# Kernel optimization log

Measured on AMD Instinct MI355X. Metric: run time of the kernel, lower is better.

Reference implementation:

```python
import jax, jax.numpy as jnp
import numpy as np

N = 100000      # nodes
E = 1600000     # edges (avg degree 16)
DIN = 128
DH = 128
DOUT = 16
G = 512         # graphs in batch


def setup_inputs() -> dict:
    key = jax.random.key(0)
    ks = jax.random.split(key, 12)
    def lin(k, fan_in, shape):
        return jax.random.uniform(k, shape, jnp.float32, -1.0, 1.0) / np.sqrt(fan_in)
    return {
        "x": jax.random.normal(ks[0], (N, DIN), jnp.float32),
        "edge_index": jax.random.randint(ks[1], (2, E), 0, N, jnp.int32),
        "edge_weight": jax.random.uniform(ks[2], (E,), jnp.float32),
        "batch": jnp.sort(jax.random.randint(ks[3], (N,), 0, G, jnp.int32)),
        "W1": lin(ks[4], DIN, (DIN, DH)), "b1": jnp.zeros((DH,), jnp.float32),
        "W2": lin(ks[5], DH, (DH, DH)),  "b2": jnp.zeros((DH,), jnp.float32),
        "W3": lin(ks[6], DH, (DH, DH)),  "b3": jnp.zeros((DH,), jnp.float32),
        "Wlin": lin(ks[7], DH, (DH, DOUT)), "blin": lin(ks[8], DH, (DOUT,)),
    }


def gcn_norm(edge_index, edge_weight, num_nodes):
    # PyG gcn_norm: add self-loops (weight 1), symmetric normalization
    loop = jnp.arange(num_nodes, dtype=edge_index.dtype)
    row = jnp.concatenate([edge_index[0], loop])
    col = jnp.concatenate([edge_index[1], loop])
    ew = jnp.concatenate([edge_weight, jnp.ones((num_nodes,), edge_weight.dtype)])
    deg = jax.ops.segment_sum(ew, col, num_segments=num_nodes)
    dinv = jnp.where(deg > 0, jax.lax.rsqrt(jnp.where(deg > 0, deg, 1.0)), 0.0)
    norm = dinv[row] * ew * dinv[col]
    return row, col, norm


def gcn_conv(x, W, b, row, col, norm, num_nodes):
    h = x @ W                                   # [N, d_out]
    msg = h[row] * norm[:, None]                # gather + scale  [E+N, d_out]
    out = jax.ops.segment_sum(msg, col, num_segments=num_nodes)
    return out + b


def reference(x, edge_index, edge_weight, batch, W1, b1, W2, b2, W3, b3, Wlin, blin):
    num_nodes = x.shape[0]
    row, col, norm = gcn_norm(edge_index, edge_weight, num_nodes)
    h = jax.nn.relu(gcn_conv(x, W1, b1, row, col, norm, num_nodes))
    h = jax.nn.relu(gcn_conv(h, W2, b2, row, col, norm, num_nodes))
    h = gcn_conv(h, W3, b3, row, col, norm, num_nodes)
    # global mean pool over graphs
    sums = jax.ops.segment_sum(h, batch, num_segments=G)          # [G, DH]
    cnt = jax.ops.segment_sum(jnp.ones((num_nodes,), h.dtype), batch, num_segments=G)
    hG = sums / jnp.maximum(cnt, 1.0)[:, None]
    # dropout is identity in eval mode
    return hG @ Wlin + blin
```

## Files before the change

kernel.cpp:

```cpp
#include <hip/hip_runtime.h>
#include <hip/hip_bf16.h>

#define NB 512
#define MAXBKT 512
#define PB 4

typedef __attribute__((ext_vector_type(8))) unsigned short ushort8;
typedef __attribute__((ext_vector_type(8))) short bf16x8;
typedef __attribute__((ext_vector_type(4))) float f32x4;

__device__ __forceinline__ unsigned short f2bf(float f) {
    unsigned u = __float_as_uint(f);
    unsigned r = (u + 0x7FFF + ((u >> 16) & 1)) >> 16;
    return (unsigned short)r;
}

__global__ __launch_bounds__(256) void k_wt3_hist(const float* __restrict__ W1,
                                                  const float* __restrict__ W2,
                                                  const float* __restrict__ W3,
                                                  const float* __restrict__ Wlin,
                                                  unsigned short* __restrict__ WT1,
                                                  unsigned short* __restrict__ WT2,
                                                  unsigned short* __restrict__ WLT,
                                                  const int* __restrict__ col, int E, int e2,
                                                  int per, int* __restrict__ cnt, int nbkt) {
    int b = blockIdx.x;
    if (b < 128) {
        const float* W = (b < 64) ? W1 : W2;
        unsigned short* WT = (b < 64) ? WT1 : WT2;
        int idx = (b & 63) * 256 + threadIdx.x;
        int nn = idx >> 7, k = idx & 127;
        WT[nn * 128 + k] = f2bf(W[k * 128 + nn]);
        return;
    }
    if (b < 136) {
        int idx = (b - 128) * 256 + threadIdx.x;
        int c = idx >> 7, k = idx & 127;
        float s = 0.f;
        for (int j = 0; j < 128; ++j) s += W3[k * 128 + j] * Wlin[j * 16 + c];
        WLT[c * 128 + k] = f2bf(s);
        return;
    }
    int hb = b - 136;
    __shared__ int h[MAXBKT];
    int t = threadIdx.x;
    for (int i = t; i < nbkt; i += 256) h[i] = 0;
    __syncthreads();
    int s = hb * per, e = min(s + per, e2);
    for (int i = s + t; i < e; i += 256) {
        int dst = (i < E) ? col[i] : i - E;
        atomicAdd(&h[dst >> 8], 1);
    }
    __syncthreads();
    for (int i = t; i < nbkt; i += 256) cnt[i * NB + hb] = h[i];
}

#define SCAN_T 256
#define SCAN_E 1024

__global__ void k_scan_a(const int* __restrict__ cnt, int n,
                         int* __restrict__ outp, int* __restrict__ bsum) {
    __shared__ int s[SCAN_T];
    int t = threadIdx.x, b = blockIdx.x;
    int base = b * SCAN_E + t * 4;
    int c0 = (base + 0 < n) ? cnt[base + 0] : 0;
    int c1 = (base + 1 < n) ? cnt[base + 1] : 0;
    int c2 = (base + 2 < n) ? cnt[base + 2] : 0;
    int c3 = (base + 3 < n) ? cnt[base + 3] : 0;
    int tsum = c0 + c1 + c2 + c3;
    s[t] = tsum; __syncthreads();
    for (int off = 1; off < SCAN_T; off <<= 1) {
        int v = (t >= off) ? s[t - off] : 0;
        __syncthreads();
        s[t] += v;
        __syncthreads();
    }
    int excl = s[t] - tsum;
    if (base + 0 < n) outp[base + 0] = excl;
    if (base + 1 < n) outp[base + 1] = excl + c0;
    if (base + 2 < n) outp[base + 2] = excl + c0 + c1;
    if (base + 3 < n) outp[base + 3] = excl + c0 + c1 + c2;
    if (t == 0) bsum[b] = s[SCAN_T - 1];
}

__global__ __launch_bounds__(256) void k_scan_b(int* __restrict__ bsum, int nb) {
    __shared__ int s[256];
    int t = threadIdx.x;
    int v = (t < nb) ? bsum[t] : 0;
    s[t] = v; __syncthreads();
    for (int off = 1; off < 256; off <<= 1) {
        int u = (t >= off) ? s[t - off] : 0;
        __syncthreads();
        s[t] += u;
        __syncthreads();
    }
    if (t < nb) bsum[t] = s[t] - v;
}

__global__ __launch_bounds__(256) void k_scatter1(const int* __restrict__ row,
                                                  const int* __restrict__ col,
                                                  const float* __restrict__ ew,
                                                  int E, int e2, int per,
                                                  const int* __restrict__ S,
                                                  const int* __restrict__ bsum,
                                                  uint2* __restrict__ csrR, int nbkt) {
    __shared__ int cur[MAXBKT];
    int t = threadIdx.x;
    for (int i = t; i < nbkt; i += 256) {
        int idx = i * NB + blockIdx.x;
        cur[i] = S[idx] + bsum[idx >> 10];
    }
    __syncthreads();
    int s = blockIdx.x * per, e = min(s + per, e2);
    for (int i = s + t; i < e; i += 256) {
        int src, dst; float w;
        if (i < E) { src = row[i]; dst = col[i]; w = ew[i]; }
        else       { src = dst = i - E; w = 1.0f; }
        int slot = atomicAdd(&cur[dst >> 8], 1);
        csrR[slot] = make_uint2(((unsigned)src << 8) | (unsigned)(dst & 255),
                                __float_as_uint(w));
    }
}

__global__ __launch_bounds__(256) void k_build(const uint2* __restrict__ csrR,
                                               const int* __restrict__ S,
                                               const int* __restrict__ bsum,
                                               int n, int e2,
                                               float2* __restrict__ csrF,
                                               float* __restrict__ dinv,
                                               int* __restrict__ rowptr, int nbkt) {
    __shared__ int   cnt[256];
    __shared__ float wsm[256];
    __shared__ int   off[256];
    __shared__ float dvs[256];
    __shared__ int   curs[256];
    int b = blockIdx.x, t = threadIdx.x;
    cnt[t] = 0; wsm[t] = 0.f;
    __syncthreads();
    int i0 = b * NB;
    int base = S[i0] + bsum[i0 >> 10];
    int end;
    if (b + 1 < nbkt) { int i1 = (b + 1) * NB; end = S[i1] + bsum[i1 >> 10]; }
    else end = e2;
    for (int i = base + t; i < end; i += 256) {
        uint2 r = csrR[i];
        int d = r.x & 255;
        atomicAdd(&cnt[d], 1);
        atomicAdd(&wsm[d], __uint_as_float(r.y));
    }
    __syncthreads();
    int   myc = cnt[t];
    float w   = wsm[t];
    float dv  = (w > 0.f) ? rsqrtf(w) : 0.f;
    dvs[t] = dv;
    off[t] = myc;
    __syncthreads();
    for (int o = 1; o < 256; o <<= 1) {
        int v = (t >= o) ? off[t - o] : 0;
        __syncthreads();
        off[t] += v;
        __syncthreads();
    }
    int excl = off[t] - myc;
    int node = b * 256 + t;
    if (node < n) { dinv[node] = dv; rowptr[node] = base + excl; }
    if (b == nbkt - 1 && t == 0) rowptr[n] = e2;
    curs[t] = excl;
    __syncthreads();
    for (int i = base + t; i < end; i += 256) {
        uint2 r = csrR[i];
        int d = r.x & 255;
        int src = (int)(r.x >> 8);
        int p = base + atomicAdd(&curs[d], 1);
        csrF[p] = make_float2(__int_as_float(src), __uint_as_float(r.y) * dvs[d]);
    }
}

__global__ __launch_bounds__(256) void k_gemm_mfma(const float* __restrict__ H,
                                                   const unsigned short* __restrict__ WT,
                                                   const float* __restrict__ dinv,
                                                   unsigned short* __restrict__ O, int n) {
    int wv = threadIdx.x >> 6, lane = threadIdx.x & 63;
    int rowBase = blockIdx.x * 64 + wv * 16;
    int lr = lane & 15;
    int lk = (lane >> 4) * 8;

    int arow = min(rowBase + lr, n - 1);
    bf16x8 a[4];
#pragma unroll
    for (int kk = 0; kk < 4; ++kk) {
        const float4* p = (const float4*)&H[(size_t)arow * 128 + kk * 32 + lk];
        float4 h0 = p[0], h1 = p[1];
        bf16x8 av;
        av[0] = (short)f2bf(h0.x); av[1] = (short)f2bf(h0.y);
        av[2] = (short)f2bf(h0.z); av[3] = (short)f2bf(h0.w);
        av[4] = (short)f2bf(h1.x); av[5] = (short)f2bf(h1.y);
        av[6] = (short)f2bf(h1.z); av[7] = (short)f2bf(h1.w);
        a[kk] = av;
    }

    f32x4 acc[8] = {};
#pragma unroll
    for (int c = 0; c < 8; ++c) {
#pragma unroll
        for (int kk = 0; kk < 4; ++kk) {
            bf16x8 b = *(const bf16x8*)&WT[(size_t)(c * 16 + lr) * 128 + kk * 32 + lk];
            acc[c] = __builtin_amdgcn_mfma_f32_16x16x32_bf16(a[kk], b, acc[c], 0, 0, 0);
        }
    }

#pragma unroll
    for (int r = 0; r < 4; ++r) {
        int node = rowBase + (lane >> 4) * 4 + r;
        if (node < n) {
            float sc = dinv[node];
#pragma unroll
            for (int c = 0; c < 8; ++c)
                O[(size_t)node * 128 + c * 16 + lr] = f2bf(acc[c][r] * sc);
        }
    }
}

#define AGG_BODY(BIAS)                                                          \
    int t = threadIdx.x;                                                        \
    int wv = t >> 6, lane = t & 63;                                             \
    int g = lane >> 4, sl = lane & 15;                                          \
    int node = blockIdx.x * 16 + wv * 4 + g;                                    \
    int s = 0, e = 0;                                                           \
    if (node < n) { s = rowptr[node]; e = rowptr[node + 1]; }                   \
    float a0 = 0.f, a1 = 0.f, a2 = 0.f, a3 = 0.f,                               \
          a4 = 0.f, a5 = 0.f, a6 = 0.f, a7 = 0.f;                               \
    int i = s;                                                                  \
    for (; i + 2 <= e; i += 2) {                                                \
        float2 p0 = csr[i], p1 = csr[i + 1];                                    \
        uint4 v0 = Hw[(size_t)__float_as_int(p0.x) * 16 + sl];                  \
        uint4 v1 = Hw[(size_t)__float_as_int(p1.x) * 16 + sl];                  \
        FMA8(v0, p0.y); FMA8(v1, p1.y);                                         \
    }                                                                           \
    if (i < e) {                                                                \
        float2 pp = csr[i];                                                     \
        uint4 v = Hw[(size_t)__float_as_int(pp.x) * 16 + sl];                   \
        FMA8(v, pp.y);                                                          \
    }                                                                           \
    const float4* b4 = (const float4*)&(BIAS)[sl * 8];                          \
    float4 bb0 = b4[0], bb1 = b4[1];                                            \
    a0 = fmaxf(a0 + bb0.x, 0.f); a1 = fmaxf(a1 + bb0.y, 0.f);                   \
    a2 = fmaxf(a2 + bb0.z, 0.f); a3 = fmaxf(a3 + bb0.w, 0.f);                   \
    a4 = fmaxf(a4 + bb1.x, 0.f); a5 = fmaxf(a5 + bb1.y, 0.f);                   \
    a6 = fmaxf(a6 + bb1.z, 0.f); a7 = fmaxf(a7 + bb1.w, 0.f);                   \
    ushort8 o;                                                                  \
    o[0] = f2bf(a0); o[1] = f2bf(a1); o[2] = f2bf(a2); o[3] = f2bf(a3);         \
    o[4] = f2bf(a4); o[5] = f2bf(a5); o[6] = f2bf(a6); o[7] = f2bf(a7);         \
    *(ushort8*)&lds[wv * 4 + g][sl * 8] = o;                                    \
    __syncthreads();

#define FMA8(V, W8) do {                                              \
    float _w = (W8);                                                  \
    a0 += __uint_as_float((V).x << 16) * _w;                          \
    a1 += __uint_as_float((V).x & 0xFFFF0000u) * _w;                  \
    a2 += __uint_as_float((V).y << 16) * _w;                          \
    a3 += __uint_as_float((V).y & 0xFFFF0000u) * _w;                  \
    a4 += __uint_as_float((V).z << 16) * _w;                          \
    a5 += __uint_as_float((V).z & 0xFFFF0000u) * _w;                  \
    a6 += __uint_as_float((V).w << 16) * _w;                          \
    a7 += __uint_as_float((V).w & 0xFFFF0000u) * _w;                  \
} while (0)

__global__ __launch_bounds__(256) void k_agg_gemm(const uint4* __restrict__ Hw,
                                                  const int* __restrict__ rowptr,
                                                  const float2* __restrict__ csr,
                                                  const float* __restrict__ bias,
                                                  const unsigned short* __restrict__ WT,
                                                  const float* __restrict__ dinv,
                                                  unsigned short* __restrict__ O, int n) {
    __shared__ __align__(16) unsigned short lds[16][132];
    AGG_BODY(bias)
    int lr = lane & 15;
    int lk = (lane >> 4) * 8;
    bf16x8 a[4];
#pragma unroll
    for (int kk = 0; kk < 4; ++kk)
        a[kk] = *(const bf16x8*)&lds[lr][kk * 32 + lk];
    f32x4 acc[2] = {};
#pragma unroll
    for (int c2 = 0; c2 < 2; ++c2) {
        int c = wv * 2 + c2;
#pragma unroll
        for (int kk = 0; kk < 4; ++kk) {
            bf16x8 b = *(const bf16x8*)&WT[(size_t)(c * 16 + lr) * 128 + kk * 32 + lk];
            acc[c2] = __builtin_amdgcn_mfma_f32_16x16x32_bf16(a[kk], b, acc[c2], 0, 0, 0);
        }
    }
#pragma unroll
    for (int r = 0; r < 4; ++r) {
        int n2 = blockIdx.x * 16 + (lane >> 4) * 4 + r;
        if (n2 < n) {
            float sc = dinv[n2];
            O[(size_t)n2 * 128 + (wv * 2 + 0) * 16 + lr] = f2bf(acc[0][r] * sc);
            O[(size_t)n2 * 128 + (wv * 2 + 1) * 16 + lr] = f2bf(acc[1][r] * sc);
        }
    }
}

__global__ __launch_bounds__(256) void k_agg_gemmP(const uint4* __restrict__ Hw,
                                                   const int* __restrict__ rowptr,
                                                   const float2* __restrict__ csr,
                                                   const float* __restrict__ bias,
                                                   const unsigned short* __restrict__ WLT,
                                                   const float* __restrict__ dinv,
                                                   float* __restrict__ P, int n) {
    __shared__ __align__(16) unsigned short lds[16][132];
    AGG_BODY(bias)
    if (wv == 0) {
        int lr = lane & 15;
        int lk = (lane >> 4) * 8;
        f32x4 acc = {};
#pragma unroll
        for (int kk = 0; kk < 4; ++kk) {
            bf16x8 a = *(const bf16x8*)&lds[lr][kk * 32 + lk];
            bf16x8 b = *(const bf16x8*)&WLT[(size_t)lr * 128 + kk * 32 + lk];
            acc = __builtin_amdgcn_mfma_f32_16x16x32_bf16(a, b, acc, 0, 0, 0);
        }
#pragma unroll
        for (int r = 0; r < 4; ++r) {
            int n2 = blockIdx.x * 16 + (lane >> 4) * 4 + r;
            if (n2 < n) P[(size_t)n2 * 16 + lr] = acc[r] * dinv[n2];
        }
    }
}
#undef FMA8
#undef AGG_BODY

__device__ __forceinline__ int lower_bound_i(const int* a, int n, int key) {
    int lo = 0, hi = n;
    while (lo < hi) { int mid = (lo + hi) >> 1; if (a[mid] < key) lo = mid + 1; else hi = mid; }
    return lo;
}

__global__ __launch_bounds__(256) void k_agg_pool(const float4* __restrict__ P4,
                                                  const int* __restrict__ rowptr,
                                                  const float2* __restrict__ csr,
                                                  const int* __restrict__ batch,
                                                  int n, float* __restrict__ partial) {
    int g = blockIdx.x >> 2, part = blockIdx.x & (PB - 1);
    int start = lower_bound_i(batch, n, g);
    int end   = lower_bound_i(batch, n, g + 1);
    int cn = end - start;
    int ns = start + (cn * part) / PB;
    int ne = start + (cn * (part + 1)) / PB;
    int es = rowptr[ns], ee = rowptr[ne];
    int t = threadIdx.x, grp = t >> 2, sl4 = t & 3;
    float a0 = 0.f, a1 = 0.f, a2 = 0.f, a3 = 0.f;
    int i = es + grp;
    for (; i + 64 < ee; i += 128) {
        float2 p0 = csr[i], p1 = csr[i + 64];
        float4 v0 = P4[(size_t)__float_as_int(p0.x) * 4 + sl4];
        float4 v1 = P4[(size_t)__float_as_int(p1.x) * 4 + sl4];
        a0 += v0.x * p0.y; a1 += v0.y * p0.y; a2 += v0.z * p0.y; a3 += v0.w * p0.y;
        a0 += v1.x * p1.y; a1 += v1.y * p1.y; a2 += v1.z * p1.y; a3 += v1.w * p1.y;
    }
    if (i < ee) {
        float2 pp = csr[i];
        float4 v = P4[(size_t)__float_as_int(pp.x) * 4 + sl4];
        a0 += v.x * pp.y; a1 += v.y * pp.y; a2 += v.z * pp.y; a3 += v.w * pp.y;
    }
    __shared__ float red[64][20];
    *(float4*)&red[grp][sl4 * 4] = make_float4(a0, a1, a2, a3);
    __syncthreads();
    if (t < 16) {
        float s = 0.f;
        for (int k2 = 0; k2 < 64; ++k2) s += red[k2][t];
        partial[(size_t)blockIdx.x * 16 + t] = s;
    }
}

__global__ void k_poolfin(const float* __restrict__ partial, const int* __restrict__ batch,
                          const float* __restrict__ b3, const float* __restrict__ Wlin,
                          const float* __restrict__ blin, float* __restrict__ out, int n) {
    int g = blockIdx.x, t = threadIdx.x;
    if (t >= 16) return;
    int start = lower_bound_i(batch, n, g);
    int end   = lower_bound_i(batch, n, g + 1);
    int cn = end - start;
    float s = partial[(size_t)(g * PB + 0) * 16 + t] + partial[(size_t)(g * PB + 1) * 16 + t]
            + partial[(size_t)(g * PB + 2) * 16 + t] + partial[(size_t)(g * PB + 3) * 16 + t];
    float bw = 0.f;
    for (int ch = 0; ch < 128; ++ch) bw += b3[ch] * Wlin[ch * 16 + t];
    out[g * 16 + t] = (cn > 0) ? s / (float)cn + bw + blin[t] : blin[t];
}

extern "C" void kernel_launch(void* const* d_in, const int* in_sizes, int n_in,
                              void* d_out, int out_size, void* d_ws, size_t ws_size,
                              hipStream_t stream) {
    const float* x    = (const float*)d_in[0];
    const int*   ei   = (const int*)d_in[1];
    const float* ew   = (const float*)d_in[2];
    const int*   batch= (const int*)d_in[3];
    const float* W1   = (const float*)d_in[4];
    const float* b1   = (const float*)d_in[5];
    const float* W2   = (const float*)d_in[6];
    const float* b2   = (const float*)d_in[7];
    const float* W3   = (const float*)d_in[8];
    const float* b3   = (const float*)d_in[9];
    const float* Wlin = (const float*)d_in[10];
    const float* blin = (const float*)d_in[11];
    float* out = (float*)d_out;

    int n  = in_sizes[0] / 128;
    int E  = in_sizes[2];
    int e2 = E + n;
    int G  = out_size / 16;
    const int* row = ei;
    const int* col = ei + E;

    int nbkt = (n + 255) >> 8;
    int M    = nbkt * NB;

    char* ws = (char*)d_ws;
    size_t off = 0;
    auto alloc = [&](size_t bytes) -> void* {
        void* p = ws + off;
        off = (off + bytes + 255) & ~255UL;
        return p;
    };
    size_t rawBytes = (size_t)e2 * 8;
    size_t hBytes   = (size_t)n * 128 * 2;
    void* regionA = alloc(rawBytes > hBytes ? rawBytes : hBytes);
    uint2*  csrR  = (uint2*)regionA;
    unsigned short* bufM2 = (unsigned short*)regionA;
    unsigned short* bufM1 = (unsigned short*)alloc((size_t)n * 128 * 2);
    float2* csrF  = (float2*)alloc((size_t)e2 * 8);
    int*    cntA  = (int*)  alloc((size_t)M * 4);
    int*    S     = (int*)  alloc((size_t)M * 4);
    int*    bsum  = (int*)  alloc(4096);
    float*  dinv  = (float*)alloc((size_t)n * 4);
    int*    rowptr= (int*)  alloc((size_t)(n + 1) * 4);
    unsigned short* WT1 = (unsigned short*)alloc(128 * 128 * 2);
    unsigned short* WT2 = (unsigned short*)alloc(128 * 128 * 2);
    unsigned short* WLT = (unsigned short*)alloc(16 * 128 * 2);
    float*  P       = (float*)alloc((size_t)n * 16 * 4);
    float*  partial = (float*)alloc((size_t)G * PB * 16 * 4);
    (void)ws_size;

    int per = (e2 + NB - 1) / NB;
    int nbScan = (M + SCAN_E - 1) / SCAN_E;

    k_wt3_hist<<<136 + NB, 256, 0, stream>>>(W1, W2, W3, Wlin, WT1, WT2, WLT,
                                             col, E, e2, per, cntA, nbkt);
    k_scan_a<<<nbScan, SCAN_T, 0, stream>>>(cntA, M, S, bsum);
    k_scan_b<<<1, 256, 0, stream>>>(bsum, nbScan);
    k_scatter1<<<NB, 256, 0, stream>>>(row, col, ew, E, e2, per, S, bsum, csrR, nbkt);
    k_build<<<nbkt, 256, 0, stream>>>(csrR, S, bsum, n, e2, csrF, dinv, rowptr, nbkt);

    int gb = (n + 63) / 64;
    int ab = (n + 15) / 16;
    k_gemm_mfma<<<gb, 256, 0, stream>>>(x, WT1, dinv, bufM1, n);
    k_agg_gemm<<<ab, 256, 0, stream>>>((const uint4*)bufM1, rowptr, csrF, b1, WT2, dinv, bufM2, n);
    k_agg_gemmP<<<ab, 256, 0, stream>>>((const uint4*)bufM2, rowptr, csrF, b2, WLT, dinv, P, n);
    k_agg_pool<<<G * PB, 256, 0, stream>>>((const float4*)P, rowptr, csrF, batch, n, partial);
    k_poolfin<<<G, 64, 0, stream>>>(partial, batch, b3, Wlin, blin, out, n);
}
```

Baseline: 279.5 us.

## Restructure aggregation to 4 lanes per node with per-wave GEMM tiles

The aggregation kernels now give each node 4 lanes, each loading 64 contiguous bytes of the neighbor row, instead of 16 lanes with 16 bytes each. A block now covers 64 nodes, 16 per wave. Each wave stages its own 16-row tile in LDS and runs the full 128-column MFMA GEMM on it, so the block-wide __syncthreads is gone and every wave does GEMM work. The aim is more nodes in flight per wave and less block-level synchronization. The cost is 32 float accumulators per lane, which raises register pressure, and more serial per-lane edge loops that are sensitive to degree imbalance.

```diff
diff --git a/kernel.cpp b/kernel.cpp
--- a/kernel.cpp
+++ b/kernel.cpp
@@ -221,49 +221,51 @@
     }
 }
 
-#define AGG_BODY(BIAS)                                                          \
-    int t = threadIdx.x;                                                        \
-    int wv = t >> 6, lane = t & 63;                                             \
-    int g = lane >> 4, sl = lane & 15;                                          \
-    int node = blockIdx.x * 16 + wv * 4 + g;                                    \
-    int s = 0, e = 0;                                                           \
-    if (node < n) { s = rowptr[node]; e = rowptr[node + 1]; }                   \
-    float a0 = 0.f, a1 = 0.f, a2 = 0.f, a3 = 0.f,                               \
-          a4 = 0.f, a5 = 0.f, a6 = 0.f, a7 = 0.f;                               \
-    int i = s;                                                                  \
-    for (; i + 2 <= e; i += 2) {                                                \
-        float2 p0 = csr[i], p1 = csr[i + 1];                                    \
-        uint4 v0 = Hw[(size_t)__float_as_int(p0.x) * 16 + sl];                  \
-        uint4 v1 = Hw[(size_t)__float_as_int(p1.x) * 16 + sl];                  \
-        FMA8(v0, p0.y); FMA8(v1, p1.y);                                         \
-    }                                                                           \
-    if (i < e) {                                                                \
-        float2 pp = csr[i];                                                     \
-        uint4 v = Hw[(size_t)__float_as_int(pp.x) * 16 + sl];                   \
-        FMA8(v, pp.y);                                                          \
-    }                                                                           \
-    const float4* b4 = (const float4*)&(BIAS)[sl * 8];                          \
-    float4 bb0 = b4[0], bb1 = b4[1];                                            \
-    a0 = fmaxf(a0 + bb0.x, 0.f); a1 = fmaxf(a1 + bb0.y, 0.f);                   \
-    a2 = fmaxf(a2 + bb0.z, 0.f); a3 = fmaxf(a3 + bb0.w, 0.f);                   \
-    a4 = fmaxf(a4 + bb1.x, 0.f); a5 = fmaxf(a5 + bb1.y, 0.f);                   \
-    a6 = fmaxf(a6 + bb1.z, 0.f); a7 = fmaxf(a7 + bb1.w, 0.f);                   \
-    ushort8 o;                                                                  \
-    o[0] = f2bf(a0); o[1] = f2bf(a1); o[2] = f2bf(a2); o[3] = f2bf(a3);         \
-    o[4] = f2bf(a4); o[5] = f2bf(a5); o[6] = f2bf(a6); o[7] = f2bf(a7);         \
-    *(ushort8*)&lds[wv * 4 + g][sl * 8] = o;                                    \
-    __syncthreads();
-
-#define FMA8(V, W8) do {                                              \
-    float _w = (W8);                                                  \
-    a0 += __uint_as_float((V).x << 16) * _w;                          \
-    a1 += __uint_as_float((V).x & 0xFFFF0000u) * _w;                  \
-    a2 += __uint_as_float((V).y << 16) * _w;                          \
-    a3 += __uint_as_float((V).y & 0xFFFF0000u) * _w;                  \
-    a4 += __uint_as_float((V).z << 16) * _w;                          \
-    a5 += __uint_as_float((V).z & 0xFFFF0000u) * _w;                  \
-    a6 += __uint_as_float((V).w << 16) * _w;                          \
-    a7 += __uint_as_float((V).w & 0xFFFF0000u) * _w;                  \
+#define AGG_WAVE_BODY(BIAS)                                                       \
+    int t = threadIdx.x;                                                          \
+    int wv = t >> 6, lane = t & 63;                                               \
+    int nl = lane >> 2, cl = lane & 3;                                            \
+    int node = blockIdx.x * 64 + wv * 16 + nl;                                    \
+    int s = 0, e = 0;                                                             \
+    if (node < n) { s = rowptr[node]; e = rowptr[node + 1]; }                     \
+    float a[32];                                                                  \
+    _Pragma("unroll")                                                             \
+    for (int j = 0; j < 32; ++j) a[j] = 0.f;                                      \
+    for (int i = s; i < e; ++i) {                                                 \
+        float2 pp = csr[i];                                                       \
+        const uint4* rb = &Hw[(size_t)__float_as_int(pp.x) * 16 + cl * 4];        \
+        uint4 v0 = rb[0], v1 = rb[1], v2 = rb[2], v3 = rb[3];                     \
+        float w = pp.y;                                                           \
+        ACC8(0, v0, w); ACC8(1, v1, w); ACC8(2, v2, w); ACC8(3, v3, w);           \
+    }                                                                             \
+    _Pragma("unroll")                                                             \
+    for (int q = 0; q < 4; ++q) {                                                 \
+        const float4* bq = (const float4*)&(BIAS)[32 * cl + q * 8];               \
+        float4 b0 = bq[0], b1 = bq[1];                                            \
+        a[q*8+0] = fmaxf(a[q*8+0] + b0.x, 0.f);                                   \
+        a[q*8+1] = fmaxf(a[q*8+1] + b0.y, 0.f);                                   \
+        a[q*8+2] = fmaxf(a[q*8+2] + b0.z, 0.f);                                   \
+        a[q*8+3] = fmaxf(a[q*8+3] + b0.w, 0.f);                                   \
+        a[q*8+4] = fmaxf(a[q*8+4] + b1.x, 0.f);                                   \
+        a[q*8+5] = fmaxf(a[q*8+5] + b1.y, 0.f);                                   \
+        a[q*8+6] = fmaxf(a[q*8+6] + b1.z, 0.f);                                   \
+        a[q*8+7] = fmaxf(a[q*8+7] + b1.w, 0.f);                                   \
+        ushort8 o;                                                                \
+        _Pragma("unroll")                                                         \
+        for (int j = 0; j < 8; ++j) o[j] = f2bf(a[q*8+j]);                        \
+        *(ushort8*)&lds[wv][nl][32 * cl + q * 8] = o;                             \
+    }                                                                             \
+    __builtin_amdgcn_sched_barrier(0);
+
+#define ACC8(q, V, W) do {                                            \
+    a[(q)*8+0] += __uint_as_float((V).x << 16) * (W);                 \
+    a[(q)*8+1] += __uint_as_float((V).x & 0xFFFF0000u) * (W);         \
+    a[(q)*8+2] += __uint_as_float((V).y << 16) * (W);                 \
+    a[(q)*8+3] += __uint_as_float((V).y & 0xFFFF0000u) * (W);         \
+    a[(q)*8+4] += __uint_as_float((V).z << 16) * (W);                 \
+    a[(q)*8+5] += __uint_as_float((V).z & 0xFFFF0000u) * (W);         \
+    a[(q)*8+6] += __uint_as_float((V).w << 16) * (W);                 \
+    a[(q)*8+7] += __uint_as_float((V).w & 0xFFFF0000u) * (W);         \
 } while (0)
 
 __global__ __launch_bounds__(256) void k_agg_gemm(const uint4* __restrict__ Hw,
@@ -273,31 +275,31 @@
                                                   const unsigned short* __restrict__ WT,
                                                   const float* __restrict__ dinv,
                                                   unsigned short* __restrict__ O, int n) {
-    __shared__ __align__(16) unsigned short lds[16][132];
-    AGG_BODY(bias)
+    __shared__ __align__(16) unsigned short lds[4][16][132];
+    AGG_WAVE_BODY(bias)
     int lr = lane & 15;
     int lk = (lane >> 4) * 8;
-    bf16x8 a[4];
+    bf16x8 av[4];
 #pragma unroll
     for (int kk = 0; kk < 4; ++kk)
-        a[kk] = *(const bf16x8*)&lds[lr][kk * 32 + lk];
-    f32x4 acc[2] = {};
-#pragma unroll
-    for (int c2 = 0; c2 < 2; ++c2) {
-        int c = wv * 2 + c2;
+        av[kk] = *(const bf16x8*)&lds[wv][lr][kk * 32 + lk];
+    f32x4 acc[8] = {};
+#pragma unroll
+    for (int c = 0; c < 8; ++c) {
 #pragma unroll
         for (int kk = 0; kk < 4; ++kk) {
             bf16x8 b = *(const bf16x8*)&WT[(size_t)(c * 16 + lr) * 128 + kk * 32 + lk];
-            acc[c2] = __builtin_amdgcn_mfma_f32_16x16x32_bf16(a[kk], b, acc[c2], 0, 0, 0);
+            acc[c] = __builtin_amdgcn_mfma_f32_16x16x32_bf16(av[kk], b, acc[c], 0, 0, 0);
         }
     }
 #pragma unroll
     for (int r = 0; r < 4; ++r) {
-        int n2 = blockIdx.x * 16 + (lane >> 4) * 4 + r;
+        int n2 = blockIdx.x * 64 + wv * 16 + (lane >> 4) * 4 + r;
         if (n2 < n) {
             float sc = dinv[n2];
-            O[(size_t)n2 * 128 + (wv * 2 + 0) * 16 + lr] = f2bf(acc[0][r] * sc);
-            O[(size_t)n2 * 128 + (wv * 2 + 1) * 16 + lr] = f2bf(acc[1][r] * sc);
+#pragma unroll
+            for (int c = 0; c < 8; ++c)
+                O[(size_t)n2 * 128 + c * 16 + lr] = f2bf(acc[c][r] * sc);
         }
     }
 }
@@ -309,27 +311,25 @@
                                                    const unsigned short* __restrict__ WLT,
                                                    const float* __restrict__ dinv,
                                                    float* __restrict__ P, int n) {
-    __shared__ __align__(16) unsigned short lds[16][132];
-    AGG_BODY(bias)
-    if (wv == 0) {
-        int lr = lane & 15;
-        int lk = (lane >> 4) * 8;
-        f32x4 acc = {};
-#pragma unroll
-        for (int kk = 0; kk < 4; ++kk) {
-            bf16x8 a = *(const bf16x8*)&lds[lr][kk * 32 + lk];
-            bf16x8 b = *(const bf16x8*)&WLT[(size_t)lr * 128 + kk * 32 + lk];
-            acc = __builtin_amdgcn_mfma_f32_16x16x32_bf16(a, b, acc, 0, 0, 0);
-        }
-#pragma unroll
-        for (int r = 0; r < 4; ++r) {
-            int n2 = blockIdx.x * 16 + (lane >> 4) * 4 + r;
-            if (n2 < n) P[(size_t)n2 * 16 + lr] = acc[r] * dinv[n2];
-        }
-    }
-}
-#undef FMA8
-#undef AGG_BODY
+    __shared__ __align__(16) unsigned short lds[4][16][132];
+    AGG_WAVE_BODY(bias)
+    int lr = lane & 15;
+    int lk = (lane >> 4) * 8;
+    f32x4 acc = {};
+#pragma unroll
+    for (int kk = 0; kk < 4; ++kk) {
+        bf16x8 av = *(const bf16x8*)&lds[wv][lr][kk * 32 + lk];
+        bf16x8 b = *(const bf16x8*)&WLT[(size_t)lr * 128 + kk * 32 + lk];
+        acc = __builtin_amdgcn_mfma_f32_16x16x32_bf16(av, b, acc, 0, 0, 0);
+    }
+#pragma unroll
+    for (int r = 0; r < 4; ++r) {
+        int n2 = blockIdx.x * 64 + wv * 16 + (lane >> 4) * 4 + r;
+        if (n2 < n) P[(size_t)n2 * 16 + lr] = acc[r] * dinv[n2];
+    }
+}
+#undef ACC8
+#undef AGG_WAVE_BODY
 
 __device__ __forceinline__ int lower_bound_i(const int* a, int n, int key) {
     int lo = 0, hi = n;
@@ -453,10 +453,9 @@
     k_build<<<nbkt, 256, 0, stream>>>(csrR, S, bsum, n, e2, csrF, dinv, rowptr, nbkt);
 
     int gb = (n + 63) / 64;
-    int ab = (n + 15) / 16;
     k_gemm_mfma<<<gb, 256, 0, stream>>>(x, WT1, dinv, bufM1, n);
-    k_agg_gemm<<<ab, 256, 0, stream>>>((const uint4*)bufM1, rowptr, csrF, b1, WT2, dinv, bufM2, n);
-    k_agg_gemmP<<<ab, 256, 0, stream>>>((const uint4*)bufM2, rowptr, csrF, b2, WLT, dinv, P, n);
+    k_agg_gemm<<<gb, 256, 0, stream>>>((const uint4*)bufM1, rowptr, csrF, b1, WT2, dinv, bufM2, n);
+    k_agg_gemmP<<<gb, 256, 0, stream>>>((const uint4*)bufM2, rowptr, csrF, b2, WLT, dinv, P, n);
     k_agg_pool<<<G * PB, 256, 0, stream>>>((const float4*)P, rowptr, csrF, batch, n, partial);
     k_poolfin<<<G, 64, 0, stream>>>(partial, batch, b3, Wlin, blin, out, n);
 }
```

Measured after the change: 318.1 us. 1.14x slower.

## Sort nodes by degree to balance work in aggregation kernels

Applied to the files above, without the earlier changes.

Adds a counting sort that buckets nodes by in-degree (capped at 63) into a permutation array. The two fused aggregate+GEMM kernels then process nodes in permutation order, so each wavefront's four node groups have similar edge counts and fewer lanes sit idle on divergent loop lengths. The cost is four extra small launches (histogram, two scan passes, scatter), an extra indirection per node, and scattered output writes plus less locality in CSR reads.

```diff
diff --git a/kernel.cpp b/kernel.cpp
--- a/kernel.cpp
+++ b/kernel.cpp
@@ -4,6 +4,8 @@
 #define NB 512
 #define MAXBKT 512
 #define PB 4
+#define DB 64
+#define DGB 256
 
 typedef __attribute__((ext_vector_type(8))) unsigned short ushort8;
 typedef __attribute__((ext_vector_type(8))) short bf16x8;
@@ -176,6 +178,40 @@
     }
 }
 
+__global__ __launch_bounds__(256) void k_deg_hist(const int* __restrict__ rowptr, int n,
+                                                  int per, int* __restrict__ cnt2) {
+    __shared__ int h[DB];
+    int t = threadIdx.x, b = blockIdx.x;
+    if (t < DB) h[t] = 0;
+    __syncthreads();
+    int s = b * per, e = min(s + per, n);
+    for (int i = s + t; i < e; i += 256) {
+        int d = min(rowptr[i + 1] - rowptr[i], DB - 1);
+        atomicAdd(&h[d], 1);
+    }
+    __syncthreads();
+    if (t < DB) cnt2[t * DGB + b] = h[t];
+}
+
+__global__ __launch_bounds__(256) void k_perm_scatter(const int* __restrict__ rowptr, int n,
+                                                      int per, const int* __restrict__ S2,
+                                                      const int* __restrict__ bsum2,
+                                                      int* __restrict__ perm) {
+    __shared__ int cur[DB];
+    int t = threadIdx.x, b = blockIdx.x;
+    if (t < DB) {
+        int idx = t * DGB + b;
+        cur[t] = S2[idx] + bsum2[idx >> 10];
+    }
+    __syncthreads();
+    int s = b * per, e = min(s + per, n);
+    for (int i = s + t; i < e; i += 256) {
+        int d = min(rowptr[i + 1] - rowptr[i], DB - 1);
+        int slot = atomicAdd(&cur[d], 1);
+        perm[slot] = i;
+    }
+}
+
 __global__ __launch_bounds__(256) void k_gemm_mfma(const float* __restrict__ H,
                                                    const unsigned short* __restrict__ WT,
                                                    const float* __restrict__ dinv,
@@ -225,9 +261,9 @@
     int t = threadIdx.x;                                                        \
     int wv = t >> 6, lane = t & 63;                                             \
     int g = lane >> 4, sl = lane & 15;                                          \
-    int node = blockIdx.x * 16 + wv * 4 + g;                                    \
+    int slot = blockIdx.x * 16 + wv * 4 + g;                                    \
     int s = 0, e = 0;                                                           \
-    if (node < n) { s = rowptr[node]; e = rowptr[node + 1]; }                   \
+    if (slot < n) { int nd = perm[slot]; s = rowptr[nd]; e = rowptr[nd + 1]; }  \
     float a0 = 0.f, a1 = 0.f, a2 = 0.f, a3 = 0.f,                               \
           a4 = 0.f, a5 = 0.f, a6 = 0.f, a7 = 0.f;                               \
     int i = s;                                                                  \
@@ -268,6 +304,7 @@
 
 __global__ __launch_bounds__(256) void k_agg_gemm(const uint4* __restrict__ Hw,
                                                   const int* __restrict__ rowptr,
+                                                  const int* __restrict__ perm,
                                                   const float2* __restrict__ csr,
                                                   const float* __restrict__ bias,
                                                   const unsigned short* __restrict__ WT,
@@ -293,8 +330,9 @@
     }
 #pragma unroll
     for (int r = 0; r < 4; ++r) {
-        int n2 = blockIdx.x * 16 + (lane >> 4) * 4 + r;
-        if (n2 < n) {
+        int slot2 = blockIdx.x * 16 + (lane >> 4) * 4 + r;
+        if (slot2 < n) {
+            int n2 = perm[slot2];
             float sc = dinv[n2];
             O[(size_t)n2 * 128 + (wv * 2 + 0) * 16 + lr] = f2bf(acc[0][r] * sc);
             O[(size_t)n2 * 128 + (wv * 2 + 1) * 16 + lr] = f2bf(acc[1][r] * sc);
@@ -304,6 +342,7 @@
 
 __global__ __launch_bounds__(256) void k_agg_gemmP(const uint4* __restrict__ Hw,
                                                    const int* __restrict__ rowptr,
+                                                   const int* __restrict__ perm,
                                                    const float2* __restrict__ csr,
                                                    const float* __restrict__ bias,
                                                    const unsigned short* __restrict__ WLT,
@@ -323,8 +362,11 @@
         }
 #pragma unroll
         for (int r = 0; r < 4; ++r) {
-            int n2 = blockIdx.x * 16 + (lane >> 4) * 4 + r;
-            if (n2 < n) P[(size_t)n2 * 16 + lr] = acc[r] * dinv[n2];
+            int slot2 = blockIdx.x * 16 + (lane >> 4) * 4 + r;
+            if (slot2 < n) {
+                int n2 = perm[slot2];
+                P[(size_t)n2 * 16 + lr] = acc[r] * dinv[n2];
+            }
         }
     }
 }
@@ -415,6 +457,7 @@
 
     int nbkt = (n + 255) >> 8;
     int M    = nbkt * NB;
+    int M2   = DB * DGB;
 
     char* ws = (char*)d_ws;
     size_t off = 0;
@@ -435,6 +478,10 @@
     int*    bsum  = (int*)  alloc(4096);
     float*  dinv  = (float*)alloc((size_t)n * 4);
     int*    rowptr= (int*)  alloc((size_t)(n + 1) * 4);
+    int*    cnt2  = (int*)  alloc((size_t)M2 * 4);
+    int*    S2    = (int*)  alloc((size_t)M2 * 4);
+    int*    bsum2 = (int*)  alloc(4096);
+    int*    perm  = (int*)  alloc((size_t)n * 4);
     unsigned short* WT1 = (unsigned short*)alloc(128 * 128 * 2);
     unsigned short* WT2 = (unsigned short*)alloc(128 * 128 * 2);
     unsigned short* WLT = (unsigned short*)alloc(16 * 128 * 2);
@@ -443,7 +490,9 @@
     (void)ws_size;
 
     int per = (e2 + NB - 1) / NB;
+    int per2 = (n + DGB - 1) / DGB;
     int nbScan = (M + SCAN_E - 1) / SCAN_E;
+    int nbScan2 = (M2 + SCAN_E - 1) / SCAN_E;
 
     k_wt3_hist<<<136 + NB, 256, 0, stream>>>(W1, W2, W3, Wlin, WT1, WT2, WLT,
                                              col, E, e2, per, cntA, nbkt);
@@ -452,11 +501,16 @@
     k_scatter1<<<NB, 256, 0, stream>>>(row, col, ew, E, e2, per, S, bsum, csrR, nbkt);
     k_build<<<nbkt, 256, 0, stream>>>(csrR, S, bsum, n, e2, csrF, dinv, rowptr, nbkt);
 
+    k_deg_hist<<<DGB, 256, 0, stream>>>(rowptr, n, per2, cnt2);
+    k_scan_a<<<nbScan2, SCAN_T, 0, stream>>>(cnt2, M2, S2, bsum2);
+    k_scan_b<<<1, 256, 0, stream>>>(bsum2, nbScan2);
+    k_perm_scatter<<<DGB, 256, 0, stream>>>(rowptr, n, per2, S2, bsum2, perm);
+
     int gb = (n + 63) / 64;
     int ab = (n + 15) / 16;
     k_gemm_mfma<<<gb, 256, 0, stream>>>(x, WT1, dinv, bufM1, n);
-    k_agg_gemm<<<ab, 256, 0, stream>>>((const uint4*)bufM1, rowptr, csrF, b1, WT2, dinv, bufM2, n);
-    k_agg_gemmP<<<ab, 256, 0, stream>>>((const uint4*)bufM2, rowptr, csrF, b2, WLT, dinv, P, n);
+    k_agg_gemm<<<ab, 256, 0, stream>>>((const uint4*)bufM1, rowptr, perm, csrF, b1, WT2, dinv, bufM2, n);
+    k_agg_gemmP<<<ab, 256, 0, stream>>>((const uint4*)bufM2, rowptr, perm, csrF, b2, WLT, dinv, P, n);
     k_agg_pool<<<G * PB, 256, 0, stream>>>((const float4*)P, rowptr, csrF, batch, n, partial);
     k_poolfin<<<G, 64, 0, stream>>>(partial, batch, b3, Wlin, blin, out, n);
 }
```

After: 283.3 us. About the same (+1.4%).

## Sort nodes by degree within buckets to balance aggregation wavefronts

Applied to the files above, without the earlier changes.

k_build now counting-sorts each 256-node bucket by in-degree (capped at 63) and writes a permutation array. The two aggregation kernels process nodes in permuted order, so the four 16-lane groups in a wavefront get similar edge counts and lanes idle less on divergent loop trip counts. The cost is an extra scan and atomics in k_build, one more indirection per node, and scattered output rows, which hurt write coalescing and locality.

```diff
diff --git a/kernel.cpp b/kernel.cpp
--- a/kernel.cpp
+++ b/kernel.cpp
@@ -128,12 +128,14 @@
                                                int n, int e2,
                                                float2* __restrict__ csrF,
                                                float* __restrict__ dinv,
-                                               int* __restrict__ rowptr, int nbkt) {
+                                               int* __restrict__ rowptr,
+                                               int* __restrict__ perm, int nbkt) {
     __shared__ int   cnt[256];
     __shared__ float wsm[256];
     __shared__ int   off[256];
     __shared__ float dvs[256];
     __shared__ int   curs[256];
+    __shared__ int   h64[64];
     int b = blockIdx.x, t = threadIdx.x;
     cnt[t] = 0; wsm[t] = 0.f;
     __syncthreads();
@@ -163,7 +165,8 @@
     }
     int excl = off[t] - myc;
     int node = b * 256 + t;
-    if (node < n) { dinv[node] = dv; rowptr[node] = base + excl; }
+    bool valid = node < n;
+    if (valid) { dinv[node] = dv; rowptr[node] = base + excl; }
     if (b == nbkt - 1 && t == 0) rowptr[n] = e2;
     curs[t] = excl;
     __syncthreads();
@@ -173,6 +176,26 @@
         int src = (int)(r.x >> 8);
         int p = base + atomicAdd(&curs[d], 1);
         csrF[p] = make_float2(__int_as_float(src), __uint_as_float(r.y) * dvs[d]);
+    }
+    if (t < 64) h64[t] = 0;
+    __syncthreads();
+    int db = min(myc, 63);
+    if (valid) atomicAdd(&h64[db], 1);
+    __syncthreads();
+    int hv = (t < 64) ? h64[t] : 0;
+    off[t] = hv;
+    __syncthreads();
+    for (int o = 1; o < 64; o <<= 1) {
+        int u = (t >= o && t < 64) ? off[t - o] : 0;
+        __syncthreads();
+        if (t < 64) off[t] += u;
+        __syncthreads();
+    }
+    if (t < 64) h64[t] = off[t] - hv;
+    __syncthreads();
+    if (valid) {
+        int slot = atomicAdd(&h64[db], 1);
+        perm[b * 256 + slot] = node;
     }
 }
 
@@ -225,9 +248,9 @@
     int t = threadIdx.x;                                                        \
     int wv = t >> 6, lane = t & 63;                                             \
     int g = lane >> 4, sl = lane & 15;                                          \
-    int node = blockIdx.x * 16 + wv * 4 + g;                                    \
+    int slot = blockIdx.x * 16 + wv * 4 + g;                                    \
     int s = 0, e = 0;                                                           \
-    if (node < n) { s = rowptr[node]; e = rowptr[node + 1]; }                   \
+    if (slot < n) { int nd = perm[slot]; s = rowptr[nd]; e = rowptr[nd + 1]; }  \
     float a0 = 0.f, a1 = 0.f, a2 = 0.f, a3 = 0.f,                               \
           a4 = 0.f, a5 = 0.f, a6 = 0.f, a7 = 0.f;                               \
     int i = s;                                                                  \
@@ -268,6 +291,7 @@
 
 __global__ __launch_bounds__(256) void k_agg_gemm(const uint4* __restrict__ Hw,
                                                   const int* __restrict__ rowptr,
+                                                  const int* __restrict__ perm,
                                                   const float2* __restrict__ csr,
                                                   const float* __restrict__ bias,
                                                   const unsigned short* __restrict__ WT,
@@ -293,8 +317,9 @@
     }
 #pragma unroll
     for (int r = 0; r < 4; ++r) {
-        int n2 = blockIdx.x * 16 + (lane >> 4) * 4 + r;
-        if (n2 < n) {
+        int slot2 = blockIdx.x * 16 + (lane >> 4) * 4 + r;
+        if (slot2 < n) {
+            int n2 = perm[slot2];
             float sc = dinv[n2];
             O[(size_t)n2 * 128 + (wv * 2 + 0) * 16 + lr] = f2bf(acc[0][r] * sc);
             O[(size_t)n2 * 128 + (wv * 2 + 1) * 16 + lr] = f2bf(acc[1][r] * sc);
@@ -304,6 +329,7 @@
 
 __global__ __launch_bounds__(256) void k_agg_gemmP(const uint4* __restrict__ Hw,
                                                    const int* __restrict__ rowptr,
+                                                   const int* __restrict__ perm,
                                                    const float2* __restrict__ csr,
                                                    const float* __restrict__ bias,
                                                    const unsigned short* __restrict__ WLT,
@@ -323,8 +349,11 @@
         }
 #pragma unroll
         for (int r = 0; r < 4; ++r) {
-            int n2 = blockIdx.x * 16 + (lane >> 4) * 4 + r;
-            if (n2 < n) P[(size_t)n2 * 16 + lr] = acc[r] * dinv[n2];
+            int slot2 = blockIdx.x * 16 + (lane >> 4) * 4 + r;
+            if (slot2 < n) {
+                int n2 = perm[slot2];
+                P[(size_t)n2 * 16 + lr] = acc[r] * dinv[n2];
+            }
         }
     }
 }
@@ -435,6 +464,7 @@
     int*    bsum  = (int*)  alloc(4096);
     float*  dinv  = (float*)alloc((size_t)n * 4);
     int*    rowptr= (int*)  alloc((size_t)(n + 1) * 4);
+    int*    perm  = (int*)  alloc((size_t)nbkt * 256 * 4);
     unsigned short* WT1 = (unsigned short*)alloc(128 * 128 * 2);
     unsigned short* WT2 = (unsigned short*)alloc(128 * 128 * 2);
     unsigned short* WLT = (unsigned short*)alloc(16 * 128 * 2);
@@ -450,13 +480,13 @@
     k_scan_a<<<nbScan, SCAN_T, 0, stream>>>(cntA, M, S, bsum);
     k_scan_b<<<1, 256, 0, stream>>>(bsum, nbScan);
     k_scatter1<<<NB, 256, 0, stream>>>(row, col, ew, E, e2, per, S, bsum, csrR, nbkt);
-    k_build<<<nbkt, 256, 0, stream>>>(csrR, S, bsum, n, e2, csrF, dinv, rowptr, nbkt);
+    k_build<<<nbkt, 256, 0, stream>>>(csrR, S, bsum, n, e2, csrF, dinv, rowptr, perm, nbkt);
 
     int gb = (n + 63) / 64;
     int ab = (n + 15) / 16;
     k_gemm_mfma<<<gb, 256, 0, stream>>>(x, WT1, dinv, bufM1, n);
-    k_agg_gemm<<<ab, 256, 0, stream>>>((const uint4*)bufM1, rowptr, csrF, b1, WT2, dinv, bufM2, n);
-    k_agg_gemmP<<<ab, 256, 0, stream>>>((const uint4*)bufM2, rowptr, csrF, b2, WLT, dinv, P, n);
+    k_agg_gemm<<<ab, 256, 0, stream>>>((const uint4*)bufM1, rowptr, perm, csrF, b1, WT2, dinv, bufM2, n);
+    k_agg_gemmP<<<ab, 256, 0, stream>>>((const uint4*)bufM2, rowptr, perm, csrF, b2, WLT, dinv, P, n);
     k_agg_pool<<<G * PB, 256, 0, stream>>>((const float4*)P, rowptr, csrF, batch, n, partial);
     k_poolfin<<<G, 64, 0, stream>>>(partial, batch, b3, Wlin, blin, out, n);
 }
```

New measurement: 305.3 us. 9.2% more time.
